# Performance work log

Measured on AMD Instinct MI355X. Metric: run time of the kernel, lower is better.

## Reference

```python
import jax, jax.numpy as jnp
import numpy as np

B, D_IN, N_EXP, D_EXP, TOP_K = 8192, 1024, 8, 1024, 2


def setup_inputs() -> dict:
    key = jax.random.key(0)
    ks = jax.random.split(key, 6)
    s_in = 1.0 / np.sqrt(D_IN)
    s_exp = 1.0 / np.sqrt(D_EXP)
    return {
        "x": jax.random.normal(ks[0], (B, D_IN), jnp.float32),
        "gate_w": jax.random.normal(ks[1], (D_IN, N_EXP), jnp.float32) * s_in,
        "w1": jax.random.normal(ks[2], (N_EXP, D_IN, D_EXP), jnp.float32) * s_in,
        "b1": jax.random.normal(ks[3], (N_EXP, D_EXP), jnp.float32) * 0.01,
        "w2": jax.random.normal(ks[4], (N_EXP, D_EXP, D_EXP), jnp.float32) * s_exp,
        "b2": jax.random.normal(ks[5], (N_EXP, D_EXP), jnp.float32) * 0.01,
    }


def _moe(x, gate_w, w1, b1, w2, b2):
    # Gating: top-k sparse softmax over expert logits.
    gate_logits = x @ gate_w                          # (B, E)
    top_vals, top_idx = jax.lax.top_k(gate_logits, TOP_K)  # (B, K)
    # softmax over only the top-k logits == softmax of -inf-scattered logits
    top_w = jax.nn.softmax(top_vals, axis=-1)          # (B, K)
    gate_weights = jnp.zeros_like(gate_logits).at[
        jnp.arange(x.shape[0])[:, None], top_idx
    ].set(top_w)                                       # (B, E)
    # Dense all-expert MLP (matches torch.stack over experts).
    h = jax.nn.gelu(jnp.einsum("bd,edf->ebf", x, w1) + b1[:, None, :],
                    approximate=False)                 # (E, B, F)
    expert_outs = jnp.einsum("ebf,efg->ebg", h, w2) + b2[:, None, :]  # (E, B, G)
    output = jnp.einsum("be,ebg->bg", gate_weights, expert_outs)      # (B, G)
    return output, gate_weights


def reference(x, gate_w, w1, b1, w2, b2):
    return _moe(x, gate_w, w1, b1, w2, b2)
```

## Files before the change

kernel.cpp:

```cpp
#include <hip/hip_runtime.h>
#include <math.h>
#include <stdint.h>


#define NTOK   8192
#define DIN    1024
#define NEXP   8
#define DEXP   1024
#define MAXROWS 17408
#define MAXTILES 136

typedef __bf16 bf16x8_t __attribute__((ext_vector_type(8)));
typedef float f32x4 __attribute__((ext_vector_type(4)));

__device__ __forceinline__ unsigned short f2bf(float f) {
  union { float f; unsigned int u; } v; v.f = f;
  unsigned int u = v.u;
  u += 0x7fffu + ((u >> 16) & 1u);
  return (unsigned short)(u >> 16);
}

__device__ __forceinline__ float bf2f(unsigned short s) {
  union { unsigned int u; float f; } v; v.u = ((unsigned int)s) << 16;
  return v.f;
}

__device__ __forceinline__ void async16(const void* g, void* l) {
  __builtin_amdgcn_global_load_lds((const __attribute__((address_space(1))) void*)g,
                                   (__attribute__((address_space(3))) void*)l, 16, 0, 0);
}

__device__ __forceinline__ float gelu_fast(float v) {
  float u = v * (1.5957691216057308f + 0.07135481627f * v * v);
  return v * (1.0f / (1.0f + __expf(-u)));
}

__global__ __launch_bounds__(256) void prep_kernel(const float* __restrict__ x,
                                                   const float* __restrict__ gw,
                                                   const float* __restrict__ w1,
                                                   const float* __restrict__ w2,
                                                   unsigned short* __restrict__ xbf,
                                                   unsigned short* __restrict__ w1T,
                                                   unsigned short* __restrict__ w2T,
                                                   float* __restrict__ outGate,
                                                   int* __restrict__ topE,
                                                   float* __restrict__ topW,
                                                   int* __restrict__ rowTok) {
  __shared__ float tile[64][68];
  int b = blockIdx.x;
  int tid = threadIdx.x;
  if (b < 4096) {
    int z = b >> 8;
    const float* src = (z < 8) ? w1 : w2;
    unsigned short* dst = (z < 8) ? w1T : w2T;
    int e = z & 7;
    int idx = b & 255, kt = idx >> 4, nt = idx & 15;
    const float* s = src + (size_t)e * DIN * DEXP + (size_t)kt * 64 * 1024 + nt * 64;
    unsigned short* d = dst + (size_t)e * DIN * DEXP + (size_t)nt * 64 * 1024 + kt * 64;
    int c4 = (tid & 15) * 4, r0 = tid >> 4;
    #pragma unroll
    for (int p = 0; p < 4; ++p) {
      int r = r0 + p * 16;
      *(float4*)&tile[r][c4] = *(const float4*)(s + (size_t)r * 1024 + c4);
    }
    __syncthreads();
    #pragma unroll
    for (int p = 0; p < 4; ++p) {
      int nr = r0 + p * 16;
      ushort4 o;
      o.x = f2bf(tile[c4 + 0][nr]);
      o.y = f2bf(tile[c4 + 1][nr]);
      o.z = f2bf(tile[c4 + 2][nr]);
      o.w = f2bf(tile[c4 + 3][nr]);
      *(ushort4*)(d + (size_t)nr * 1024 + c4) = o;
    }
  } else if (b < 6144) {
    int lane = tid & 63, wv = tid >> 6;
    int t = (b - 4096) * 4 + wv;
    const float4* xr = (const float4*)(x + (size_t)t * 1024);
    ushort4* xo = (ushort4*)(xbf + (size_t)t * 1024);
    double acc[NEXP];
    #pragma unroll
    for (int e = 0; e < NEXP; ++e) acc[e] = 0.0;
    #pragma unroll
    for (int j = 0; j < 4; ++j) {
      int q = lane + 64 * j;
      float4 v = xr[q];
      ushort4 r;
      r.x = f2bf(v.x); r.y = f2bf(v.y); r.z = f2bf(v.z); r.w = f2bf(v.w);
      xo[q] = r;
      float vv[4] = {v.x, v.y, v.z, v.w};
      #pragma unroll
      for (int m = 0; m < 4; ++m) {
        int k = q * 4 + m;
        float4 g0 = *(const float4*)(gw + k * 8);
        float4 g1 = *(const float4*)(gw + k * 8 + 4);
        double xv = (double)vv[m];
        acc[0] += xv * (double)g0.x; acc[1] += xv * (double)g0.y;
        acc[2] += xv * (double)g0.z; acc[3] += xv * (double)g0.w;
        acc[4] += xv * (double)g1.x; acc[5] += xv * (double)g1.y;
        acc[6] += xv * (double)g1.z; acc[7] += xv * (double)g1.w;
      }
    }
    #pragma unroll
    for (int off = 32; off > 0; off >>= 1) {
      #pragma unroll
      for (int e = 0; e < NEXP; ++e) acc[e] += __shfl_xor(acc[e], off);
    }
    if (lane == 0) {
      int e0 = 0; double v0 = acc[0];
      #pragma unroll
      for (int e = 1; e < NEXP; ++e) if (acc[e] > v0) { v0 = acc[e]; e0 = e; }
      int e1 = -1; double v1 = -1e300;
      #pragma unroll
      for (int e = 0; e < NEXP; ++e) if (e != e0 && acc[e] > v1) { v1 = acc[e]; e1 = e; }
      float ex = expf((float)(v1 - v0));
      float inv = 1.0f / (1.0f + ex);
      float w0 = inv, w1v = ex * inv;
      float g8[8];
      #pragma unroll
      for (int e = 0; e < NEXP; ++e) g8[e] = 0.f;
      g8[e0] = w0; g8[e1] = w1v;
      float4* gp = (float4*)(outGate + t * 8);
      gp[0] = *(float4*)&g8[0];
      gp[1] = *(float4*)&g8[4];
      topE[t * 2 + 0] = e0; topE[t * 2 + 1] = e1;
      topW[t * 2 + 0] = w0; topW[t * 2 + 1] = w1v;
    }
  } else {
    int base = (b - 6144) * 1024 + tid * 4;
    int4 m1 = make_int4(-1, -1, -1, -1);
    *(int4*)(rowTok + base) = m1;
  }
}

__global__ __launch_bounds__(1024) void slot_kernel(const int* __restrict__ topE,
                                                    int* __restrict__ topRow,
                                                    int* __restrict__ rowTok,
                                                    int* __restrict__ tileExpert,
                                                    int* __restrict__ tileRowBase) {
  __shared__ int wtot[16][NEXP];
  __shared__ int wbase[16][NEXP];
  __shared__ int soff[NEXP];
  int tid = threadIdx.x, lane = tid & 63, wv = tid >> 6;
  int a0 = tid * 16;
  unsigned long long pk = 0ull;
  int cnt[NEXP];
  #pragma unroll
  for (int e = 0; e < NEXP; ++e) cnt[e] = 0;
  for (int i = 0; i < 16; ++i) {
    int e = topE[a0 + i];
    pk |= (unsigned long long)e << (i * 4);
    cnt[e]++;
  }
  int excl[NEXP];
  #pragma unroll
  for (int e = 0; e < NEXP; ++e) {
    int v = cnt[e], sum = v;
    #pragma unroll
    for (int d = 1; d < 64; d <<= 1) {
      int u = __shfl_up(sum, d);
      if (lane >= d) sum += u;
    }
    excl[e] = sum - v;
    if (lane == 63) wtot[wv][e] = sum;
  }
  __syncthreads();
  if (tid == 0) {
    int counts[NEXP];
    for (int e = 0; e < NEXP; ++e) {
      int s = 0;
      for (int w = 0; w < 16; ++w) { wbase[w][e] = s; s += wtot[w][e]; }
      counts[e] = s;
    }
    int row = 0, tile = 0;
    for (int e = 0; e < NEXP; ++e) {
      soff[e] = row;
      int nt = (counts[e] + 127) >> 7;
      for (int i = 0; i < nt; ++i) { tileExpert[tile] = e; tileRowBase[tile] = row + i * 128; ++tile; }
      row += nt << 7;
    }
    for (; tile < MAXTILES; ++tile) tileExpert[tile] = -1;
  }
  __syncthreads();
  int base[NEXP], run[NEXP];
  #pragma unroll
  for (int e = 0; e < NEXP; ++e) { base[e] = soff[e] + wbase[wv][e] + excl[e]; run[e] = 0; }
  for (int i = 0; i < 16; ++i) {
    int e = (int)((pk >> (i * 4)) & 7ull);
    int row = base[e] + run[e]++;
    rowTok[row] = (a0 + i) >> 1;
    topRow[a0 + i] = row;
  }
}

__global__ __launch_bounds__(256) void gemm1_kernel(const unsigned short* __restrict__ xbf,
                                                    const unsigned short* __restrict__ w1T,
                                                    const float* __restrict__ b1,
                                                    const int* __restrict__ tileExpert,
                                                    const int* __restrict__ tileRowBase,
                                                    const int* __restrict__ rowTok,
                                                    unsigned short* __restrict__ h) {
  int tileId = blockIdx.x;
  int e = tileExpert[tileId];
  if (e < 0) return;
  int rowBase = tileRowBase[tileId];
  int n0 = blockIdx.y * 128;
  __shared__ __align__(16) unsigned short sm[128 * 64 * 2];
  unsigned short* sA = sm;
  unsigned short* sB = sm + 128 * 64;
  int tid = threadIdx.x, lane = tid & 63, wv = tid >> 6;
  int srow = tid >> 3;
  int scolSw = (((tid & 7) ^ ((tid >> 3) & 7)) * 8);
  int tok[4];
  #pragma unroll
  for (int i = 0; i < 4; ++i) {
    int tk = rowTok[rowBase + srow + i * 32];
    tok[i] = tk < 0 ? 0 : tk;
  }
  const unsigned short* Bmat = w1T + (size_t)e * DIN * DEXP;
  int wm = ((tid >> 6) & 1) * 64, wn = (tid >> 7) * 64;
  int rsel = lane & 15, q = lane >> 4;
  int rk = rsel & 7;
  f32x4 acc[4][4] = {};
  for (int kk = 0; kk < DIN; kk += 64) {
    #pragma unroll
    for (int i = 0; i < 4; ++i) {
      int abase = __builtin_amdgcn_readfirstlane((wv * 8 + i * 32) * 128);
      async16(xbf + (size_t)tok[i] * 1024 + kk + scolSw, (char*)sm + abase);
      async16(Bmat + (size_t)(n0 + srow + i * 32) * 1024 + kk + scolSw,
              (char*)sm + abase + 16384);
    }
    __syncthreads();
    #pragma unroll
    for (int ks = 0; ks < 64; ks += 32) {
      int co = (((ks >> 3) + q) ^ rk) * 8;
      bf16x8_t af[4], bfr[4];
      #pragma unroll
      for (int mi = 0; mi < 4; ++mi)
        af[mi] = *(const bf16x8_t*)&sA[(wm + mi * 16 + rsel) * 64 + co];
      #pragma unroll
      for (int ni = 0; ni < 4; ++ni)
        bfr[ni] = *(const bf16x8_t*)&sB[(wn + ni * 16 + rsel) * 64 + co];
      #pragma unroll
      for (int mi = 0; mi < 4; ++mi)
        #pragma unroll
        for (int ni = 0; ni < 4; ++ni)
          acc[mi][ni] = __builtin_amdgcn_mfma_f32_16x16x32_bf16(af[mi], bfr[ni], acc[mi][ni], 0, 0, 0);
    }
    __syncthreads();
  }
  float b1v[4];
  int quad = lane >> 4;
  #pragma unroll
  for (int ni = 0; ni < 4; ++ni) b1v[ni] = b1[e * 1024 + n0 + wn + ni * 16 + rsel];
  #pragma unroll
  for (int mi = 0; mi < 4; ++mi)
    #pragma unroll
    for (int ni = 0; ni < 4; ++ni)
      #pragma unroll
      for (int r = 0; r < 4; ++r) {
        int m = wm + mi * 16 + quad * 4 + r;
        int n = wn + ni * 16 + rsel;
        sm[m * 128 + n] = f2bf(gelu_fast(acc[mi][ni][r] + b1v[ni]));
      }
  __syncthreads();
  #pragma unroll
  for (int i = 0; i < 8; ++i) {
    int idx = i * 2048 + tid * 8;
    int m = idx >> 7, c = idx & 127;
    int g = rowBase + m;
    *(uint4*)(h + (size_t)g * 1024 + n0 + c) = *(const uint4*)&sm[idx];
  }
}

__global__ __launch_bounds__(256) void gemm2_kernel(const unsigned short* __restrict__ h,
                                                    const unsigned short* __restrict__ w2T,
                                                    const float* __restrict__ b2,
                                                    const int* __restrict__ tileExpert,
                                                    const int* __restrict__ tileRowBase,
                                                    unsigned short* __restrict__ y) {
  int tileId = blockIdx.x;
  int e = tileExpert[tileId];
  if (e < 0) return;
  int rowBase = tileRowBase[tileId];
  int n0 = blockIdx.y * 128;
  __shared__ __align__(16) unsigned short sm[128 * 64 * 2];
  unsigned short* sA = sm;
  unsigned short* sB = sm + 128 * 64;
  int tid = threadIdx.x, lane = tid & 63, wv = tid >> 6;
  int srow = tid >> 3;
  int scolSw = (((tid & 7) ^ ((tid >> 3) & 7)) * 8);
  const unsigned short* Bmat = w2T + (size_t)e * DEXP * DEXP;
  int wm = ((tid >> 6) & 1) * 64, wn = (tid >> 7) * 64;
  int rsel = lane & 15, q = lane >> 4;
  int rk = rsel & 7;
  f32x4 acc[4][4] = {};
  for (int kk = 0; kk < DEXP; kk += 64) {
    #pragma unroll
    for (int i = 0; i < 4; ++i) {
      int abase = __builtin_amdgcn_readfirstlane((wv * 8 + i * 32) * 128);
      async16(h + (size_t)(rowBase + srow + i * 32) * 1024 + kk + scolSw, (char*)sm + abase);
      async16(Bmat + (size_t)(n0 + srow + i * 32) * 1024 + kk + scolSw,
              (char*)sm + abase + 16384);
    }
    __syncthreads();
    #pragma unroll
    for (int ks = 0; ks < 64; ks += 32) {
      int co = (((ks >> 3) + q) ^ rk) * 8;
      bf16x8_t af[4], bfr[4];
      #pragma unroll
      for (int mi = 0; mi < 4; ++mi)
        af[mi] = *(const bf16x8_t*)&sA[(wm + mi * 16 + rsel) * 64 + co];
      #pragma unroll
      for (int ni = 0; ni < 4; ++ni)
        bfr[ni] = *(const bf16x8_t*)&sB[(wn + ni * 16 + rsel) * 64 + co];
      #pragma unroll
      for (int mi = 0; mi < 4; ++mi)
        #pragma unroll
        for (int ni = 0; ni < 4; ++ni)
          acc[mi][ni] = __builtin_amdgcn_mfma_f32_16x16x32_bf16(af[mi], bfr[ni], acc[mi][ni], 0, 0, 0);
    }
    __syncthreads();
  }
  float b2v[4];
  int quad = lane >> 4;
  #pragma unroll
  for (int ni = 0; ni < 4; ++ni) b2v[ni] = b2[e * 1024 + n0 + wn + ni * 16 + rsel];
  #pragma unroll
  for (int mi = 0; mi < 4; ++mi)
    #pragma unroll
    for (int ni = 0; ni < 4; ++ni)
      #pragma unroll
      for (int r = 0; r < 4; ++r) {
        int m = wm + mi * 16 + quad * 4 + r;
        int n = wn + ni * 16 + rsel;
        sm[m * 128 + n] = f2bf(acc[mi][ni][r] + b2v[ni]);
      }
  __syncthreads();
  #pragma unroll
  for (int i = 0; i < 8; ++i) {
    int idx = i * 2048 + tid * 8;
    int m = idx >> 7, c = idx & 127;
    int g = rowBase + m;
    *(uint4*)(y + (size_t)g * 1024 + n0 + c) = *(const uint4*)&sm[idx];
  }
}

__global__ __launch_bounds__(256) void combine_kernel(const unsigned short* __restrict__ y,
                                                      const int* __restrict__ topRow,
                                                      const float* __restrict__ topW,
                                                      float* __restrict__ out) {
  int tid = threadIdx.x;
  int wv = tid >> 6, lane = tid & 63;
  int t = blockIdx.x * 4 + wv;
  int r0 = topRow[t * 2 + 0], r1 = topRow[t * 2 + 1];
  float w0 = topW[t * 2 + 0], w1 = topW[t * 2 + 1];
  const unsigned short* p0 = y + (size_t)r0 * 1024 + lane * 16;
  const unsigned short* p1 = y + (size_t)r1 * 1024 + lane * 16;
  float* op = out + (size_t)t * 1024 + lane * 16;
  #pragma unroll
  for (int hh = 0; hh < 2; ++hh) {
    union { uint4 v; unsigned short s[8]; } a, b;
    a.v = *(const uint4*)(p0 + hh * 8);
    b.v = *(const uint4*)(p1 + hh * 8);
    float o[8];
    #pragma unroll
    for (int j = 0; j < 8; ++j)
      o[j] = w0 * bf2f(a.s[j]) + w1 * bf2f(b.s[j]);
    *(float4*)(op + hh * 8) = *(float4*)&o[0];
    *(float4*)(op + hh * 8 + 4) = *(float4*)&o[4];
  }
}

extern "C" void kernel_launch(void* const* d_in, const int* in_sizes, int n_in,
                              void* d_out, int out_size, void* d_ws, size_t ws_size,
                              hipStream_t stream) {
  const float* x  = (const float*)d_in[0];
  const float* gw = (const float*)d_in[1];
  const float* w1 = (const float*)d_in[2];
  const float* b1 = (const float*)d_in[3];
  const float* w2 = (const float*)d_in[4];
  const float* b2 = (const float*)d_in[5];
  float* out = (float*)d_out;

  char* ws = (char*)d_ws;
  int* tileExpert  = (int*)ws;
  int* tileRowBase = tileExpert + MAXTILES;
  int* topE        = tileRowBase + MAXTILES;
  int* topRow      = topE + 16384;
  float* topW      = (float*)(topRow + 16384);
  int* rowTok      = (int*)(ws + (256 << 10));
  unsigned short* xbf  = (unsigned short*)(ws + (512 << 10));
  unsigned short* w1T  = xbf + (size_t)NTOK * DIN;
  unsigned short* w2T  = w1T + (size_t)NEXP * DIN * DEXP;
  unsigned short* hbuf = w2T + (size_t)NEXP * DEXP * DEXP;
  unsigned short* ybuf = hbuf + (size_t)MAXROWS * DEXP;

  prep_kernel<<<4096 + 2048 + 17, 256, 0, stream>>>(x, gw, w1, w2, xbf, w1T, w2T,
                                                    out + (size_t)NTOK * DEXP,
                                                    topE, topW, rowTok);
  slot_kernel<<<1, 1024, 0, stream>>>(topE, topRow, rowTok, tileExpert, tileRowBase);
  gemm1_kernel<<<dim3(MAXTILES, 8), 256, 0, stream>>>(xbf, w1T, b1, tileExpert, tileRowBase,
                                                      rowTok, hbuf);
  gemm2_kernel<<<dim3(MAXTILES, 8), 256, 0, stream>>>(hbuf, w2T, b2, tileExpert, tileRowBase,
                                                      ybuf);
  combine_kernel<<<NTOK / 4, 256, 0, stream>>>(ybuf, topRow, topW, out);
}
```

Before: 337.2 us.

## Spread weight transpose-casts across gate, slot and gemm1 kernels to overlap work

```diff
diff --git a/kernel.cpp b/kernel.cpp
--- a/kernel.cpp
+++ b/kernel.cpp
@@ -35,102 +35,80 @@
   return v * (1.0f / (1.0f + __expf(-u)));
 }
 
-__global__ __launch_bounds__(256) void prep_kernel(const float* __restrict__ x,
-                                                   const float* __restrict__ gw,
-                                                   const float* __restrict__ w1,
-                                                   const float* __restrict__ w2,
-                                                   unsigned short* __restrict__ xbf,
-                                                   unsigned short* __restrict__ w1T,
-                                                   unsigned short* __restrict__ w2T,
-                                                   float* __restrict__ outGate,
-                                                   int* __restrict__ topE,
-                                                   float* __restrict__ topW,
-                                                   int* __restrict__ rowTok) {
-  __shared__ float tile[64][68];
+__global__ __launch_bounds__(256) void gate_cast_kernel(const float* __restrict__ x,
+                                                        const float* __restrict__ gw,
+                                                        unsigned short* __restrict__ xbf,
+                                                        float* __restrict__ outGate,
+                                                        int* __restrict__ topE,
+                                                        float* __restrict__ topW,
+                                                        int* __restrict__ rowTok) {
   int b = blockIdx.x;
   int tid = threadIdx.x;
-  if (b < 4096) {
-    int z = b >> 8;
-    const float* src = (z < 8) ? w1 : w2;
-    unsigned short* dst = (z < 8) ? w1T : w2T;
-    int e = z & 7;
-    int idx = b & 255, kt = idx >> 4, nt = idx & 15;
-    const float* s = src + (size_t)e * DIN * DEXP + (size_t)kt * 64 * 1024 + nt * 64;
-    unsigned short* d = dst + (size_t)e * DIN * DEXP + (size_t)nt * 64 * 1024 + kt * 64;
-    int c4 = (tid & 15) * 4, r0 = tid >> 4;
-    #pragma unroll
-    for (int p = 0; p < 4; ++p) {
-      int r = r0 + p * 16;
-      *(float4*)&tile[r][c4] = *(const float4*)(s + (size_t)r * 1024 + c4);
-    }
-    __syncthreads();
-    #pragma unroll
-    for (int p = 0; p < 4; ++p) {
-      int nr = r0 + p * 16;
-      ushort4 o;
-      o.x = f2bf(tile[c4 + 0][nr]);
-      o.y = f2bf(tile[c4 + 1][nr]);
-      o.z = f2bf(tile[c4 + 2][nr]);
-      o.w = f2bf(tile[c4 + 3][nr]);
-      *(ushort4*)(d + (size_t)nr * 1024 + c4) = o;
-    }
-  } else if (b < 6144) {
-    int lane = tid & 63, wv = tid >> 6;
-    int t = (b - 4096) * 4 + wv;
-    const float4* xr = (const float4*)(x + (size_t)t * 1024);
-    ushort4* xo = (ushort4*)(xbf + (size_t)t * 1024);
-    double acc[NEXP];
-    #pragma unroll
-    for (int e = 0; e < NEXP; ++e) acc[e] = 0.0;
-    #pragma unroll
-    for (int j = 0; j < 4; ++j) {
-      int q = lane + 64 * j;
-      float4 v = xr[q];
-      ushort4 r;
-      r.x = f2bf(v.x); r.y = f2bf(v.y); r.z = f2bf(v.z); r.w = f2bf(v.w);
-      xo[q] = r;
-      float vv[4] = {v.x, v.y, v.z, v.w};
-      #pragma unroll
-      for (int m = 0; m < 4; ++m) {
-        int k = q * 4 + m;
-        float4 g0 = *(const float4*)(gw + k * 8);
-        float4 g1 = *(const float4*)(gw + k * 8 + 4);
-        double xv = (double)vv[m];
-        acc[0] += xv * (double)g0.x; acc[1] += xv * (double)g0.y;
-        acc[2] += xv * (double)g0.z; acc[3] += xv * (double)g0.w;
-        acc[4] += xv * (double)g1.x; acc[5] += xv * (double)g1.y;
-        acc[6] += xv * (double)g1.z; acc[7] += xv * (double)g1.w;
-      }
-    }
-    #pragma unroll
-    for (int off = 32; off > 0; off >>= 1) {
-      #pragma unroll
-      for (int e = 0; e < NEXP; ++e) acc[e] += __shfl_xor(acc[e], off);
-    }
-    if (lane == 0) {
-      int e0 = 0; double v0 = acc[0];
-      #pragma unroll
-      for (int e = 1; e < NEXP; ++e) if (acc[e] > v0) { v0 = acc[e]; e0 = e; }
-      int e1 = -1; double v1 = -1e300;
-      #pragma unroll
-      for (int e = 0; e < NEXP; ++e) if (e != e0 && acc[e] > v1) { v1 = acc[e]; e1 = e; }
-      float ex = expf((float)(v1 - v0));
-      float inv = 1.0f / (1.0f + ex);
-      float w0 = inv, w1v = ex * inv;
-      float g8[8];
-      #pragma unroll
-      for (int e = 0; e < NEXP; ++e) g8[e] = 0.f;
-      g8[e0] = w0; g8[e1] = w1v;
-      float4* gp = (float4*)(outGate + t * 8);
-      gp[0] = *(float4*)&g8[0];
-      gp[1] = *(float4*)&g8[4];
-      topE[t * 2 + 0] = e0; topE[t * 2 + 1] = e1;
-      topW[t * 2 + 0] = w0; topW[t * 2 + 1] = w1v;
-    }
-  } else {
-    int base = (b - 6144) * 1024 + tid * 4;
-    int4 m1 = make_int4(-1, -1, -1, -1);
-    *(int4*)(rowTok + base) = m1;
+  if (b >= 2048) {
+    int base = (b - 2048) * 1024 + tid * 4;
+    *(int4*)(rowTok + base) = make_int4(-1, -1, -1, -1);
+    return;
+  }
+  __shared__ float gwT[NEXP][1024];
+  #pragma unroll
+  for (int it = 0; it < 8; ++it) {
+    int idx = it * 256 + tid;
+    int fk = idx >> 1;
+    int e0 = (idx & 1) * 4;
+    float4 g = *(const float4*)(gw + fk * 8 + e0);
+    gwT[e0 + 0][fk] = g.x; gwT[e0 + 1][fk] = g.y;
+    gwT[e0 + 2][fk] = g.z; gwT[e0 + 3][fk] = g.w;
+  }
+  __syncthreads();
+
+  int lane = tid & 63, wv = tid >> 6;
+  int t = b * 4 + wv;
+  const float4* xr = (const float4*)(x + (size_t)t * 1024);
+  ushort4* xo = (ushort4*)(xbf + (size_t)t * 1024);
+  double acc[NEXP];
+  #pragma unroll
+  for (int e = 0; e < NEXP; ++e) acc[e] = 0.0;
+  #pragma unroll
+  for (int j = 0; j < 4; ++j) {
+    int q = lane + 64 * j;
+    float4 v = xr[q];
+    ushort4 r;
+    r.x = f2bf(v.x); r.y = f2bf(v.y); r.z = f2bf(v.z); r.w = f2bf(v.w);
+    xo[q] = r;
+    float vv[4] = {v.x, v.y, v.z, v.w};
+    #pragma unroll
+    for (int e = 0; e < NEXP; ++e) {
+      float4 g = *(const float4*)&gwT[e][4 * q];
+      acc[e] += (double)vv[0] * (double)g.x;
+      acc[e] += (double)vv[1] * (double)g.y;
+      acc[e] += (double)vv[2] * (double)g.z;
+      acc[e] += (double)vv[3] * (double)g.w;
+    }
+  }
+  #pragma unroll
+  for (int off = 32; off > 0; off >>= 1) {
+    #pragma unroll
+    for (int e = 0; e < NEXP; ++e) acc[e] += __shfl_xor(acc[e], off);
+  }
+  if (lane == 0) {
+    int e0 = 0; double v0 = acc[0];
+    #pragma unroll
+    for (int e = 1; e < NEXP; ++e) if (acc[e] > v0) { v0 = acc[e]; e0 = e; }
+    int e1 = -1; double v1 = -1e300;
+    #pragma unroll
+    for (int e = 0; e < NEXP; ++e) if (e != e0 && acc[e] > v1) { v1 = acc[e]; e1 = e; }
+    float ex = expf((float)(v1 - v0));
+    float inv = 1.0f / (1.0f + ex);
+    float w0 = inv, w1v = ex * inv;
+    float g8[8];
+    #pragma unroll
+    for (int e = 0; e < NEXP; ++e) g8[e] = 0.f;
+    g8[e0] = w0; g8[e1] = w1v;
+    float4* gp = (float4*)(outGate + t * 8);
+    gp[0] = *(float4*)&g8[0];
+    gp[1] = *(float4*)&g8[4];
+    topE[t * 2 + 0] = e0; topE[t * 2 + 1] = e1;
+    topW[t * 2 + 0] = w0; topW[t * 2 + 1] = w1v;
   }
 }
 
@@ -138,11 +116,36 @@
                                                     int* __restrict__ topRow,
                                                     int* __restrict__ rowTok,
                                                     int* __restrict__ tileExpert,
-                                                    int* __restrict__ tileRowBase) {
+                                                    int* __restrict__ tileRowBase,
+                                                    const float* __restrict__ w1,
+                                                    unsigned short* __restrict__ w1T) {
   __shared__ int wtot[16][NEXP];
   __shared__ int wbase[16][NEXP];
   __shared__ int soff[NEXP];
-  int tid = threadIdx.x, lane = tid & 63, wv = tid >> 6;
+  __shared__ float tile[64 * 65];
+  int tid = threadIdx.x;
+  if (blockIdx.x != 0) {
+    int idx = blockIdx.x - 1;
+    int e = idx >> 8, rest = idx & 255, kt = rest >> 4, nt = rest & 15;
+    const float* s = w1 + (size_t)e * DIN * DEXP + (size_t)kt * 64 * 1024 + nt * 64;
+    unsigned short* d = w1T + (size_t)e * DIN * DEXP + (size_t)nt * 64 * 1024 + kt * 64;
+    int a = tid & 15, r = tid >> 4;
+    float4 v = *(const float4*)(s + (size_t)r * 1024 + a * 4);
+    tile[r * 65 + a * 4 + 0] = v.x;
+    tile[r * 65 + a * 4 + 1] = v.y;
+    tile[r * 65 + a * 4 + 2] = v.z;
+    tile[r * 65 + a * 4 + 3] = v.w;
+    __syncthreads();
+    int nr = r;
+    ushort4 o;
+    o.x = f2bf(tile[(a * 4 + 0) * 65 + nr]);
+    o.y = f2bf(tile[(a * 4 + 1) * 65 + nr]);
+    o.z = f2bf(tile[(a * 4 + 2) * 65 + nr]);
+    o.w = f2bf(tile[(a * 4 + 3) * 65 + nr]);
+    *(ushort4*)(d + (size_t)nr * 1024 + a * 4) = o;
+    return;
+  }
+  int lane = tid & 63, wv = tid >> 6;
   int a0 = tid * 16;
   unsigned long long pk = 0ull;
   int cnt[NEXP];
@@ -173,14 +176,14 @@
       for (int w = 0; w < 16; ++w) { wbase[w][e] = s; s += wtot[w][e]; }
       counts[e] = s;
     }
-    int row = 0, tile = 0;
+    int row = 0, tile2 = 0;
     for (int e = 0; e < NEXP; ++e) {
       soff[e] = row;
       int nt = (counts[e] + 127) >> 7;
-      for (int i = 0; i < nt; ++i) { tileExpert[tile] = e; tileRowBase[tile] = row + i * 128; ++tile; }
+      for (int i = 0; i < nt; ++i) { tileExpert[tile2] = e; tileRowBase[tile2] = row + i * 128; ++tile2; }
       row += nt << 7;
     }
-    for (; tile < MAXTILES; ++tile) tileExpert[tile] = -1;
+    for (; tile2 < MAXTILES; ++tile2) tileExpert[tile2] = -1;
   }
   __syncthreads();
   int base[NEXP], run[NEXP];
@@ -197,19 +200,52 @@
 __global__ __launch_bounds__(256) void gemm1_kernel(const unsigned short* __restrict__ xbf,
                                                     const unsigned short* __restrict__ w1T,
                                                     const float* __restrict__ b1,
+                                                    const float* __restrict__ w2,
+                                                    unsigned short* __restrict__ w2T,
                                                     const int* __restrict__ tileExpert,
                                                     const int* __restrict__ tileRowBase,
                                                     const int* __restrict__ rowTok,
                                                     unsigned short* __restrict__ h) {
-  int tileId = blockIdx.x;
+  __shared__ __align__(16) unsigned short sm[128 * 64 * 2];
+  int bid = blockIdx.x;
+  int tid = threadIdx.x;
+  if (bid < 2048) {
+    float* tile = (float*)sm;
+    int e = bid >> 8, rest = bid & 255, kt = rest >> 4, nt = rest & 15;
+    const float* s = w2 + (size_t)e * DEXP * DEXP + (size_t)kt * 64 * 1024 + nt * 64;
+    unsigned short* d = w2T + (size_t)e * DEXP * DEXP + (size_t)nt * 64 * 1024 + kt * 64;
+    int a = tid & 15, r0 = tid >> 4;
+    #pragma unroll
+    for (int p = 0; p < 4; ++p) {
+      int r = r0 + p * 16;
+      float4 v = *(const float4*)(s + (size_t)r * 1024 + a * 4);
+      tile[r * 65 + a * 4 + 0] = v.x;
+      tile[r * 65 + a * 4 + 1] = v.y;
+      tile[r * 65 + a * 4 + 2] = v.z;
+      tile[r * 65 + a * 4 + 3] = v.w;
+    }
+    __syncthreads();
+    #pragma unroll
+    for (int p = 0; p < 4; ++p) {
+      int nr = r0 + p * 16;
+      ushort4 o;
+      o.x = f2bf(tile[(a * 4 + 0) * 65 + nr]);
+      o.y = f2bf(tile[(a * 4 + 1) * 65 + nr]);
+      o.z = f2bf(tile[(a * 4 + 2) * 65 + nr]);
+      o.w = f2bf(tile[(a * 4 + 3) * 65 + nr]);
+      *(ushort4*)(d + (size_t)nr * 1024 + a * 4) = o;
+    }
+    return;
+  }
+  int g = bid - 2048;
+  int tileId = g % MAXTILES;
   int e = tileExpert[tileId];
   if (e < 0) return;
   int rowBase = tileRowBase[tileId];
-  int n0 = blockIdx.y * 128;
-  __shared__ __align__(16) unsigned short sm[128 * 64 * 2];
+  int n0 = (g / MAXTILES) * 128;
   unsigned short* sA = sm;
   unsigned short* sB = sm + 128 * 64;
-  int tid = threadIdx.x, lane = tid & 63, wv = tid >> 6;
+  int lane = tid & 63, wv = tid >> 6;
   int srow = tid >> 3;
   int scolSw = (((tid & 7) ^ ((tid >> 3) & 7)) * 8);
   int tok[4];
@@ -269,8 +305,8 @@
   for (int i = 0; i < 8; ++i) {
     int idx = i * 2048 + tid * 8;
     int m = idx >> 7, c = idx & 127;
-    int g = rowBase + m;
-    *(uint4*)(h + (size_t)g * 1024 + n0 + c) = *(const uint4*)&sm[idx];
+    int gg = rowBase + m;
+    *(uint4*)(h + (size_t)gg * 1024 + n0 + c) = *(const uint4*)&sm[idx];
   }
 }
 
@@ -397,13 +433,15 @@
   unsigned short* hbuf = w2T + (size_t)NEXP * DEXP * DEXP;
   unsigned short* ybuf = hbuf + (size_t)MAXROWS * DEXP;
 
-  prep_kernel<<<4096 + 2048 + 17, 256, 0, stream>>>(x, gw, w1, w2, xbf, w1T, w2T,
-                                                    out + (size_t)NTOK * DEXP,
-                                                    topE, topW, rowTok);
-  slot_kernel<<<1, 1024, 0, stream>>>(topE, topRow, rowTok, tileExpert, tileRowBase);
-  gemm1_kernel<<<dim3(MAXTILES, 8), 256, 0, stream>>>(xbf, w1T, b1, tileExpert, tileRowBase,
-                                                      rowTok, hbuf);
-  gemm2_kernel<<<dim3(MAXTILES, 8), 256, 0, stream>>>(hbuf, w2T, b2, tileExpert, tileRowBase,
-                                                      ybuf);
+  gate_cast_kernel<<<2048 + 17, 256, 0, stream>>>(x, gw, xbf,
+                                                  out + (size_t)NTOK * DEXP,
+                                                  topE, topW, rowTok);
+  slot_kernel<<<1 + 2048, 1024, 0, stream>>>(topE, topRow, rowTok, tileExpert,
+                                             tileRowBase, w1, w1T);
+  gemm1_kernel<<<2048 + MAXTILES * 8, 256, 0, stream>>>(xbf, w1T, b1, w2, w2T,
+                                                        tileExpert, tileRowBase,
+                                                        rowTok, hbuf);
+  gemm2_kernel<<<dim3(MAXTILES, 8), 256, 0, stream>>>(hbuf, w2T, b2, tileExpert,
+                                                      tileRowBase, ybuf);
   combine_kernel<<<NTOK / 4, 256, 0, stream>>>(ybuf, topRow, topW, out);
 }
```

Measured after the change: 292.3 us. 13.3% less time.
